# Optimization experiments

Measured on AMD Instinct MI355X. Metric: run time of the kernel, lower is better.

Reference implementation:

```python
import jax, jax.numpy as jnp
import numpy as np

V, D, H, L, S_MAX, FF = 32000, 1024, 16, 6, 1024, 4096
HD = D // H
EPS = 1e-5

def _ln(x, g, b):
    mu = jnp.mean(x, axis=-1, keepdims=True)
    var = jnp.mean((x - mu) ** 2, axis=-1, keepdims=True)
    return (x - mu) * jax.lax.rsqrt(var + EPS) * g + b

def setup_inputs() -> dict:
    key = jax.random.key(0)
    ks = jax.random.split(key, 12)
    std = 0.02
    d = {}
    d['x'] = jax.random.randint(ks[0], (2, 1024), 0, V)
    d['tok_emb'] = std * jax.random.normal(ks[1], (V, D), jnp.float32)
    d['pos_emb'] = std * jax.random.normal(ks[2], (S_MAX, D), jnp.float32)
    d['ln1_g'] = jnp.ones((L, D)); d['ln1_b'] = jnp.zeros((L, D))
    d['qkv_w'] = std * jax.random.normal(ks[3], (L, 3 * D, D), jnp.float32)
    d['qkv_b'] = jnp.zeros((L, 3 * D))
    d['proj_w'] = std * jax.random.normal(ks[4], (L, D, D), jnp.float32)
    d['proj_b'] = jnp.zeros((L, D))
    d['ln2_g'] = jnp.ones((L, D)); d['ln2_b'] = jnp.zeros((L, D))
    d['fc1_w'] = std * jax.random.normal(ks[5], (L, FF, D), jnp.float32)
    d['fc1_b'] = jnp.zeros((L, FF))
    d['fc2_w'] = std * jax.random.normal(ks[6], (L, D, FF), jnp.float32)
    d['fc2_b'] = jnp.zeros((L, D))
    d['lnf_g'] = jnp.ones((D,)); d['lnf_b'] = jnp.zeros((D,))
    d['head_w'] = std * jax.random.normal(ks[7], (V, D), jnp.float32)
    return d

def _gpt(x, tok_emb, pos_emb, ln1_g, ln1_b, qkv_w, qkv_b, proj_w, proj_b,
         ln2_g, ln2_b, fc1_w, fc1_b, fc2_w, fc2_b, lnf_g, lnf_b, head_w):
    B, S = x.shape
    h = tok_emb[x] + pos_emb[:S][None]  # (B,S,D)
    scale = HD ** -0.5
    causal = jnp.tril(jnp.ones((S, S), bool))
    neg_inf = jnp.finfo(h.dtype).min

    def block(h, p):
        l1g, l1b, qw, qb, pw, pb, l2g, l2b, f1w, f1b, f2w, f2b = p
        xn = _ln(h, l1g, l1b)
        qkv = xn @ qw.T + qb  # (B,S,3D)
        qkv = qkv.reshape(B, S, 3, H, HD).transpose(2, 0, 3, 1, 4)  # (3,B,H,S,HD)
        q, k, v = qkv[0], qkv[1], qkv[2]
        scores = jnp.einsum('bhqd,bhkd->bhqk', q, k) * scale
        scores = jnp.where(causal, scores, neg_inf)
        attn = jax.nn.softmax(scores, axis=-1)
        o = jnp.einsum('bhqk,bhkd->bhqd', attn, v)
        o = o.transpose(0, 2, 1, 3).reshape(B, S, D)
        h = h + (o @ pw.T + pb)
        xn = _ln(h, l2g, l2b)
        ff = jax.nn.gelu(xn @ f1w.T + f1b, approximate=False) @ f2w.T + f2b
        return h + ff, None

    params = (ln1_g, ln1_b, qkv_w, qkv_b, proj_w, proj_b,
              ln2_g, ln2_b, fc1_w, fc1_b, fc2_w, fc2_b)
    h, _ = jax.lax.scan(block, h, params)
    h = _ln(h, lnf_g, lnf_b)
    return h @ head_w.T  # (B,S,V)

def reference(x, tok_emb, pos_emb, ln1_g, ln1_b, qkv_w, qkv_b, proj_w, proj_b,
              ln2_g, ln2_b, fc1_w, fc1_b, fc2_w, fc2_b, lnf_g, lnf_b, head_w):
    return _gpt(x, tok_emb, pos_emb, ln1_g, ln1_b, qkv_w, qkv_b, proj_w, proj_b,
                ln2_g, ln2_b, fc1_w, fc1_b, fc2_w, fc2_b, lnf_g, lnf_b, head_w)
```

## Files before the change

kernel.cpp:

```cpp
#include <hip/hip_runtime.h>

typedef unsigned short u16;
typedef unsigned int   u32;
typedef __bf16 bf16x8 __attribute__((ext_vector_type(8)));
typedef float  f32x4  __attribute__((ext_vector_type(4)));

#define DEV __device__ __forceinline__

DEV u16 f2bf(float f) {
    u32 u = __builtin_bit_cast(u32, f);
    u32 r = u + 0x7FFFu + ((u >> 16) & 1u);
    return (u16)(r >> 16);
}

DEV void gload16(const void* g, void* l) {
    __builtin_amdgcn_global_load_lds((const __attribute__((address_space(1))) void*)g,
                                     (__attribute__((address_space(3))) void*)l, 16, 0, 0);
}

DEV int xcd_swz(int bid, int nwg) {
    int q = nwg >> 3, r = nwg & 7;
    int xcd = bid & 7, idx = bid >> 3;
    return (xcd < r ? xcd * (q + 1) : r * (q + 1) + (xcd - r) * q) + idx;
}

DEV int swz(int p) {
    int m = (((p >> 7) & 1) << 6) | (((p >> 9) & 1) << 5) | (((p >> 8) & 1) << 4);
    return p ^ m;
}

__global__ void cvt_k(const float* __restrict__ src, u16* __restrict__ dst, int n4) {
    int i = blockIdx.x * blockDim.x + threadIdx.x;
    int stride = gridDim.x * blockDim.x;
    for (; i < n4; i += stride) {
        float4 v = ((const float4*)src)[i];
        ushort4 u;
        u.x = f2bf(v.x); u.y = f2bf(v.y); u.z = f2bf(v.z); u.w = f2bf(v.w);
        ((ushort4*)dst)[i] = u;
    }
}

__global__ void cvt4_k(const float* __restrict__ s0, const float* __restrict__ s1,
                       const float* __restrict__ s2, const float* __restrict__ s3,
                       u16* __restrict__ dst, int n0, int n1, int n2, int n3) {
    int i = blockIdx.x * blockDim.x + threadIdx.x;
    int stride = gridDim.x * blockDim.x;
    int t0 = n0, t1 = t0 + n1, t2 = t1 + n2, t3 = t2 + n3;
    for (; i < t3; i += stride) {
        const float* s; int j;
        if (i < t0)      { s = s0; j = i; }
        else if (i < t1) { s = s1; j = i - t0; }
        else if (i < t2) { s = s2; j = i - t1; }
        else             { s = s3; j = i - t2; }
        float4 v = ((const float4*)s)[j];
        ushort4 u;
        u.x = f2bf(v.x); u.y = f2bf(v.y); u.z = f2bf(v.z); u.w = f2bf(v.w);
        ((ushort4*)dst)[i] = u;
    }
}

__global__ void embed_k(const int* __restrict__ x, const float* __restrict__ te,
                        const float* __restrict__ pe, float* __restrict__ h) {
    int row = blockIdx.x;
    int t = threadIdx.x;
    int tok = x[row];
    int s = row & 1023;
    float4 a = ((const float4*)(te + (size_t)tok * 1024))[t];
    float4 p = ((const float4*)(pe + (size_t)s * 1024))[t];
    a.x += p.x; a.y += p.y; a.z += p.z; a.w += p.w;
    ((float4*)(h + (size_t)row * 1024))[t] = a;
}

__global__ void ln_k(const float* __restrict__ in, const float* __restrict__ g,
                     const float* __restrict__ b, u16* __restrict__ out) {
    int row = blockIdx.x;
    int t = threadIdx.x;
    float4 v = ((const float4*)(in + (size_t)row * 1024))[t];
    float s = v.x + v.y + v.z + v.w;
    float s2 = v.x * v.x + v.y * v.y + v.z * v.z + v.w * v.w;
    #pragma unroll
    for (int msk = 1; msk < 64; msk <<= 1) {
        s  += __shfl_xor(s, msk);
        s2 += __shfl_xor(s2, msk);
    }
    __shared__ float ps[4], ps2[4];
    if ((t & 63) == 0) { ps[t >> 6] = s; ps2[t >> 6] = s2; }
    __syncthreads();
    s = ps[0] + ps[1] + ps[2] + ps[3];
    s2 = ps2[0] + ps2[1] + ps2[2] + ps2[3];
    float mu = s * (1.0f / 1024.0f);
    float var = s2 * (1.0f / 1024.0f) - mu * mu;
    float rstd = rsqrtf(var + 1e-5f);
    float4 gg = ((const float4*)g)[t];
    float4 bb = ((const float4*)b)[t];
    ushort4 o;
    o.x = f2bf((v.x - mu) * rstd * gg.x + bb.x);
    o.y = f2bf((v.y - mu) * rstd * gg.y + bb.y);
    o.z = f2bf((v.z - mu) * rstd * gg.z + bb.z);
    o.w = f2bf((v.w - mu) * rstd * gg.w + bb.w);
    ((ushort4*)out)[(size_t)row * 256 + t] = o;
}

__global__ void fuse2_k(const float* __restrict__ p0, const float* __restrict__ p1,
                        const float* __restrict__ bias, float* __restrict__ h) {
    int row = blockIdx.x;
    int t = threadIdx.x;
    size_t idx = (size_t)row * 256 + t;
    float4 a = ((const float4*)p0)[idx];
    float4 b = ((const float4*)p1)[idx];
    float4 c = ((const float4*)bias)[t];
    float4 v = ((const float4*)h)[idx];
    v.x += a.x + b.x + c.x;
    v.y += a.y + b.y + c.y;
    v.z += a.z + b.z + c.z;
    v.w += a.w + b.w + c.w;
    ((float4*)h)[idx] = v;
}

template<int PH>
DEV void phase_mma(const bf16x8 (&af)[2][2], const bf16x8 (&bfr)[4][2], f32x4 (&acc)[8][4]) {
    __builtin_amdgcn_s_barrier();
    asm volatile("s_waitcnt lgkmcnt(0)" ::: "memory");
    __builtin_amdgcn_sched_barrier(0);
    __builtin_amdgcn_s_setprio(1);
    #pragma unroll
    for (int ms = 0; ms < 2; ++ms)
        #pragma unroll
        for (int nj = 0; nj < 4; ++nj)
            #pragma unroll
            for (int kk = 0; kk < 2; ++kk)
                acc[PH * 2 + ms][nj] = __builtin_amdgcn_mfma_f32_16x16x32_bf16(
                    af[ms][kk], bfr[nj][kk], acc[PH * 2 + ms][nj], 0, 0, 0);
    __builtin_amdgcn_s_setprio(0);
}

template<int PH>
DEV void read_afrags(const char* Ab, int arow, int fr, int fq, bf16x8 (&af)[2][2]) {
    #pragma unroll
    for (int ms = 0; ms < 2; ++ms)
        #pragma unroll
        for (int kk = 0; kk < 2; ++kk) {
            int lin = (arow + (PH * 2 + ms) * 16 + fr) * 128 + kk * 64 + fq * 16;
            af[ms][kk] = *(const bf16x8*)(Ab + swz(lin));
        }
}

template<int BIAS, int OUTBF>
__global__ __launch_bounds__(512, 2)
void gemm8p(const u16* __restrict__ A, const u16* __restrict__ Bw,
            const float* __restrict__ bias,
            float* __restrict__ outf, u16* __restrict__ outb,
            int M, int N, int K) {
    __shared__ char lds[131072];
    char* ldsA = lds;
    char* ldsB = lds + 65536;
    const int t = threadIdx.x;
    const int w = t >> 6, l = t & 63;
    const int fr = l & 15, fq = l >> 4;
    const int wm = w >> 2, wn = w & 3;

    int bid = blockIdx.y * gridDim.x + blockIdx.x;
    int swzb = xcd_swz(bid, gridDim.x * gridDim.y);
    const int m0 = (swzb % gridDim.x) * 256;
    const int n0 = (swzb / gridDim.x) * 256;
    const int nt = K >> 6;
    const int arow = wm * 128;

    const u16* Asrc = A + (size_t)m0 * K;
    const u16* Bsrc = Bw + (size_t)n0 * K;

    size_t o00, o01, o10, o11;
    {
        int p;
        p = 0 * 16384 + 0 * 8192 + t * 16; o00 = (size_t)(p >> 7) * K + ((swz(p) & 127) >> 1);
        p = 0 * 16384 + 1 * 8192 + t * 16; o01 = (size_t)(p >> 7) * K + ((swz(p) & 127) >> 1);
        p = 1 * 16384 + 0 * 8192 + t * 16; o10 = (size_t)(p >> 7) * K + ((swz(p) & 127) >> 1);
        p = 1 * 16384 + 1 * 8192 + t * 16; o11 = (size_t)(p >> 7) * K + ((swz(p) & 127) >> 1);
    }
    const int wb = w * 1024;

    gload16(Asrc + o00, ldsA + wb);
    gload16(Asrc + o01, ldsA + 8192 + wb);
    gload16(Asrc + o10, ldsA + 16384 + wb);
    gload16(Asrc + o11, ldsA + 16384 + 8192 + wb);
    gload16(Bsrc + o00, ldsB + wb);
    gload16(Bsrc + o01, ldsB + 8192 + wb);
    gload16(Bsrc + o10, ldsB + 16384 + wb);
    gload16(Bsrc + o11, ldsB + 16384 + 8192 + wb);
    gload16(Bsrc + o00 + 64, ldsB + 32768 + wb);
    gload16(Bsrc + o01 + 64, ldsB + 32768 + 8192 + wb);
    gload16(Bsrc + o10 + 64, ldsB + 32768 + 16384 + wb);
    gload16(Bsrc + o11 + 64, ldsB + 32768 + 16384 + 8192 + wb);
    asm volatile("s_waitcnt vmcnt(4)" ::: "memory");
    __builtin_amdgcn_s_barrier();
    __builtin_amdgcn_sched_barrier(0);

    f32x4 acc[8][4] = {};

    for (int T = 0; T < nt; ++T) {
        const char* Ab = ldsA + (T & 1) * 32768;
        const char* Bb = ldsB + (T & 1) * 32768;
        char* Anx = ldsA + ((T + 1) & 1) * 32768;
        char* Bnx = ldsB + (T & 1) * 32768;
        const bool stA = (T + 1 < nt), stB = (T + 2 < nt);
        const size_t kA = (size_t)(T + 1) * 64, kB = (size_t)(T + 2) * 64;

        bf16x8 bfr[4][2], af[2][2];

        #pragma unroll
        for (int nj = 0; nj < 4; ++nj)
            #pragma unroll
            for (int kk = 0; kk < 2; ++kk) {
                int lin = (wn * 64 + nj * 16 + fr) * 128 + kk * 64 + fq * 16;
                bfr[nj][kk] = *(const bf16x8*)(Bb + swz(lin));
            }
        read_afrags<0>(Ab, arow, fr, fq, af);
        if (stA) {
            gload16(Asrc + o00 + kA, Anx + wb);
            gload16(Asrc + o01 + kA, Anx + 8192 + wb);
        }
        phase_mma<0>(af, bfr, acc);
        __builtin_amdgcn_s_barrier();

        read_afrags<1>(Ab, arow, fr, fq, af);
        if (stA) {
            gload16(Asrc + o10 + kA, Anx + 16384 + wb);
            gload16(Asrc + o11 + kA, Anx + 16384 + 8192 + wb);
        }
        phase_mma<1>(af, bfr, acc);
        __builtin_amdgcn_s_barrier();

        read_afrags<2>(Ab, arow, fr, fq, af);
        if (stB) {
            gload16(Bsrc + o00 + kB, Bnx + wb);
            gload16(Bsrc + o01 + kB, Bnx + 8192 + wb);
        }
        phase_mma<2>(af, bfr, acc);
        __builtin_amdgcn_s_barrier();

        read_afrags<3>(Ab, arow, fr, fq, af);
        if (stB) {
            gload16(Bsrc + o10 + kB, Bnx + 16384 + wb);
            gload16(Bsrc + o11 + kB, Bnx + 16384 + 8192 + wb);
        }
        phase_mma<3>(af, bfr, acc);
        if (stB)      asm volatile("s_waitcnt vmcnt(4)" ::: "memory");
        else if (stA) asm volatile("s_waitcnt vmcnt(0)" ::: "memory");
        __builtin_amdgcn_s_barrier();
        __builtin_amdgcn_sched_barrier(0);
    }

    #pragma unroll
    for (int mi = 0; mi < 8; ++mi) {
        #pragma unroll
        for (int nj = 0; nj < 4; ++nj) {
            #pragma unroll
            for (int r = 0; r < 4; ++r) {
                int row = m0 + wm * 128 + mi * 16 + fq * 4 + r;
                int col = n0 + wn * 64 + nj * 16 + fr;
                float v = acc[mi][nj][r];
                if (BIAS) v += bias[col];
                if (OUTBF) outb[(size_t)row * N + col] = f2bf(v);
                else       outf[(size_t)row * N + col] = v;
            }
        }
    }
}

template<int BM, int BN, int BIAS, int GELU_, int RES, int OUTBF, int SPLITK>
__global__ void gemm_db(const u16* __restrict__ A, const u16* __restrict__ Bw,
                        const float* __restrict__ bias, const float* __restrict__ res,
                        float* __restrict__ outf, u16* __restrict__ outb,
                        int M, int N, int K) {
    constexpr int MR = BM / 32;
    constexpr int NR = BN / 32;
    constexpr int AL = BM / 64;
    constexpr int BL = BN / 64;
    __shared__ u16 lA[2][BM * 32];
    __shared__ u16 lB[2][BN * 32];
    const int t = threadIdx.x;
    const int w = t >> 6, l = t & 63;

    int bid = blockIdx.y * gridDim.x + blockIdx.x;
    int swzb = xcd_swz(bid, gridDim.x * gridDim.y);
    const int m0 = (swzb % gridDim.x) * BM;
    const int n0 = (swzb / gridDim.x) * BN;

    int kbase = 0, Keff = K;
    if (SPLITK) { Keff = K >> 1; kbase = blockIdx.z * Keff; }
    const int nt = Keff >> 5;

    const int wr = (w >> 1) * (BM / 2), wc = (w & 1) * (BN / 2);
    const int fr = l & 15, fq = l >> 4;
    const int g0 = w * 64 + l;

    const int srow = g0 >> 2, scol = (g0 & 3) * 8;

    f32x4 acc[MR][NR] = {};

    #pragma unroll
    for (int i = 0; i < AL; ++i)
        gload16(A + (size_t)(m0 + srow + i * 64) * K + kbase + scol, lA[0] + (srow + i * 64) * 32 + scol);
    #pragma unroll
    for (int i = 0; i < BL; ++i)
        gload16(Bw + (size_t)(n0 + srow + i * 64) * K + kbase + scol, lB[0] + (srow + i * 64) * 32 + scol);
    __syncthreads();

    for (int T = 0; T < nt; ++T) {
        const int cur = T & 1, nxt = cur ^ 1;
        if (T + 1 < nt) {
            const int kk = kbase + (T + 1) * 32;
            #pragma unroll
            for (int i = 0; i < AL; ++i)
                gload16(A + (size_t)(m0 + srow + i * 64) * K + kk + scol, lA[nxt] + (srow + i * 64) * 32 + scol);
            #pragma unroll
            for (int i = 0; i < BL; ++i)
                gload16(Bw + (size_t)(n0 + srow + i * 64) * K + kk + scol, lB[nxt] + (srow + i * 64) * 32 + scol);
        }
        bf16x8 af[MR], bfv[NR];
        #pragma unroll
        for (int mi = 0; mi < MR; ++mi)
            af[mi] = *(const bf16x8*)(lA[cur] + (wr + mi * 16 + fr) * 32 + fq * 8);
        #pragma unroll
        for (int ni = 0; ni < NR; ++ni)
            bfv[ni] = *(const bf16x8*)(lB[cur] + (wc + ni * 16 + fr) * 32 + fq * 8);
        #pragma unroll
        for (int mi = 0; mi < MR; ++mi)
            #pragma unroll
            for (int ni = 0; ni < NR; ++ni)
                acc[mi][ni] = __builtin_amdgcn_mfma_f32_16x16x32_bf16(af[mi], bfv[ni], acc[mi][ni], 0, 0, 0);
        __syncthreads();
    }

    float* op = outf;
    if (SPLITK) op = outf + (size_t)blockIdx.z * M * N;

    #pragma unroll
    for (int mi = 0; mi < MR; ++mi) {
        #pragma unroll
        for (int ni = 0; ni < NR; ++ni) {
            #pragma unroll
            for (int r = 0; r < 4; ++r) {
                int row = m0 + wr + mi * 16 + fq * 4 + r;
                int col = n0 + wc + ni * 16 + fr;
                float v = acc[mi][ni][r];
                if (BIAS) v += bias[col];
                if (GELU_) v = 0.5f * v * (1.0f + erff(v * 0.70710678118f));
                if (RES) v += res[(size_t)row * N + col];
                if (OUTBF) outb[(size_t)row * N + col] = f2bf(v);
                else       op[(size_t)row * N + col] = v;
            }
        }
    }
}

__global__ void attn_k(const u16* __restrict__ qkv, u16* __restrict__ o) {
    __shared__ u16 lK[64 * 64];
    __shared__ u16 lV[64 * 64];
    __shared__ u16 lP[4 * 16 * 64];
    const int t = threadIdx.x;
    const int w = t >> 6, l = t & 63;
    const int fr = l & 15, fq = l >> 4;

    int swzb = xcd_swz(blockIdx.x, gridDim.x);
    const int qb = 15 - (swzb & 15);
    const int hh = (swzb >> 4) & 15;
    const int b  = swzb >> 8;
    const int q0 = qb * 64;

    const u16* srcK[2];
    #pragma unroll
    for (int i = 0; i < 2; ++i) {
        int p = (t + i * 256) * 16;
        int L = swz(p);
        srcK[i] = qkv + ((size_t)(b * 1024) + (L >> 7)) * 3072 + 1024 + hh * 64 + ((L & 127) >> 1);
    }

    bf16x8 qf[2];
    {
        size_t base = ((size_t)(b * 1024) + q0 + w * 16 + fr) * 3072 + hh * 64;
        qf[0] = *(const bf16x8*)(qkv + base + fq * 8);
        qf[1] = *(const bf16x8*)(qkv + base + 32 + fq * 8);
    }

    float m_run[4], l_run[4];
    f32x4 acc_o[4] = {};
    #pragma unroll
    for (int r = 0; r < 4; ++r) { m_run[r] = -__builtin_inff(); l_run[r] = 0.0f; }

    for (int kv0 = 0; kv0 <= q0; kv0 += 64) {
        #pragma unroll
        for (int i = 0; i < 2; ++i)
            gload16(srcK[i] + (size_t)kv0 * 3072, (char*)lK + w * 1024 + i * 4096);
        #pragma unroll
        for (int i = 0; i < 2; ++i) {
            int g = t + i * 256;
            int kv = g >> 3, d0 = (g & 7) * 8;
            const u32* gv = (const u32*)(qkv + ((size_t)(b * 1024) + kv0 + kv) * 3072 + 2048 + hh * 64 + d0);
            u32 v0 = gv[0], v1 = gv[1], v2 = gv[2], v3 = gv[3];
            u16 e[8] = { (u16)v0, (u16)(v0 >> 16), (u16)v1, (u16)(v1 >> 16),
                         (u16)v2, (u16)(v2 >> 16), (u16)v3, (u16)(v3 >> 16) };
            #pragma unroll
            for (int j = 0; j < 8; ++j) {
                int pv = ((d0 + j) * 64 + kv) * 2;
                *(u16*)((char*)lV + swz(pv)) = e[j];
            }
        }
        __syncthreads();

        f32x4 accs[4] = {};
        #pragma unroll
        for (int nt = 0; nt < 4; ++nt) {
            #pragma unroll
            for (int ks = 0; ks < 2; ++ks) {
                int pk = ((nt * 16 + fr) * 64 + ks * 32 + fq * 8) * 2;
                bf16x8 kf = *(const bf16x8*)((const char*)lK + swz(pk));
                accs[nt] = __builtin_amdgcn_mfma_f32_16x16x32_bf16(qf[ks], kf, accs[nt], 0, 0, 0);
            }
        }

        float p[4][4], mx[4], rs[4];
        #pragma unroll
        for (int r = 0; r < 4; ++r) {
            int qg = q0 + w * 16 + fq * 4 + r;
            float m = -__builtin_inff();
            #pragma unroll
            for (int nt = 0; nt < 4; ++nt) {
                int kvg = kv0 + nt * 16 + fr;
                float s = (kvg <= qg) ? accs[nt][r] * 0.125f : -__builtin_inff();
                p[nt][r] = s;
                m = fmaxf(m, s);
            }
            mx[r] = m;
        }
        #pragma unroll
        for (int msk = 1; msk < 16; msk <<= 1) {
            #pragma unroll
            for (int r = 0; r < 4; ++r) mx[r] = fmaxf(mx[r], __shfl_xor(mx[r], msk));
        }
        float mnew[4], alpha[4];
        #pragma unroll
        for (int r = 0; r < 4; ++r) {
            mnew[r] = fmaxf(m_run[r], mx[r]);
            alpha[r] = __expf(m_run[r] - mnew[r]);
            float s = 0.0f;
            #pragma unroll
            for (int nt = 0; nt < 4; ++nt) {
                float pv = __expf(p[nt][r] - mnew[r]);
                p[nt][r] = pv;
                s += pv;
            }
            rs[r] = s;
        }
        #pragma unroll
        for (int msk = 1; msk < 16; msk <<= 1) {
            #pragma unroll
            for (int r = 0; r < 4; ++r) rs[r] += __shfl_xor(rs[r], msk);
        }
        #pragma unroll
        for (int r = 0; r < 4; ++r) {
            l_run[r] = l_run[r] * alpha[r] + rs[r];
            m_run[r] = mnew[r];
        }
        #pragma unroll
        for (int nt = 0; nt < 4; ++nt)
            #pragma unroll
            for (int r = 0; r < 4; ++r) acc_o[nt][r] *= alpha[r];

        #pragma unroll
        for (int nt = 0; nt < 4; ++nt)
            #pragma unroll
            for (int r = 0; r < 4; ++r) {
                int pp = (w * 1024 + (fq * 4 + r) * 64 + nt * 16 + fr) * 2;
                *(u16*)((char*)lP + swz(pp)) = f2bf(p[nt][r]);
            }
        __syncthreads();

        bf16x8 pa[2];
        #pragma unroll
        for (int ks = 0; ks < 2; ++ks) {
            int ppr = (w * 1024 + fr * 64 + ks * 32 + fq * 8) * 2;
            pa[ks] = *(const bf16x8*)((const char*)lP + swz(ppr));
        }
        #pragma unroll
        for (int nt = 0; nt < 4; ++nt) {
            #pragma unroll
            for (int ks = 0; ks < 2; ++ks) {
                int pvr = ((nt * 16 + fr) * 64 + ks * 32 + fq * 8) * 2;
                bf16x8 vf = *(const bf16x8*)((const char*)lV + swz(pvr));
                acc_o[nt] = __builtin_amdgcn_mfma_f32_16x16x32_bf16(pa[ks], vf, acc_o[nt], 0, 0, 0);
            }
        }
        __syncthreads();
    }

    #pragma unroll
    for (int nt = 0; nt < 4; ++nt) {
        #pragma unroll
        for (int r = 0; r < 4; ++r) {
            int qg = q0 + w * 16 + fq * 4 + r;
            int d = nt * 16 + fr;
            float ov = acc_o[nt][r] / l_run[r];
            o[((size_t)(b * 1024) + qg) * 1024 + hh * 64 + d] = f2bf(ov);
        }
    }
}

extern "C" void kernel_launch(void* const* d_in, const int* in_sizes, int n_in,
                              void* d_out, int out_size, void* d_ws, size_t ws_size,
                              hipStream_t stream) {
    const int*   x       = (const int*)  d_in[0];
    const float* tok_emb = (const float*)d_in[1];
    const float* pos_emb = (const float*)d_in[2];
    const float* ln1_g   = (const float*)d_in[3];
    const float* ln1_b   = (const float*)d_in[4];
    const float* qkv_w   = (const float*)d_in[5];
    const float* qkv_b   = (const float*)d_in[6];
    const float* proj_w  = (const float*)d_in[7];
    const float* proj_b  = (const float*)d_in[8];
    const float* ln2_g   = (const float*)d_in[9];
    const float* ln2_b   = (const float*)d_in[10];
    const float* fc1_w   = (const float*)d_in[11];
    const float* fc1_b   = (const float*)d_in[12];
    const float* fc2_w   = (const float*)d_in[13];
    const float* fc2_b   = (const float*)d_in[14];
    const float* lnf_g   = (const float*)d_in[15];
    const float* lnf_b   = (const float*)d_in[16];
    const float* head_w  = (const float*)d_in[17];
    float* out = (float*)d_out;

    char* ws = (char*)d_ws;
    float* h   = (float*)(ws + 0);
    u16*   xn  = (u16*)(ws + 8388608);
    u16*   qkv = (u16*)(ws + 12582912);
    u16*   ob  = (u16*)(ws + 25165824);
    u16*   ff  = (u16*)(ws + 29360128);
    u16*   wq  = (u16*)(ws + 46137344);
    float* pbuf = (float*)(ws + 12582912);

    u16* wqkv = wq;
    u16* wproj = wqkv + 3072 * 1024;
    u16* wfc1  = wproj + 1024 * 1024;
    u16* wfc2  = wfc1 + 4096 * 1024;

    const int M = 2048;

    embed_k<<<dim3(2048), 256, 0, stream>>>(x, tok_emb, pos_emb, h);

    for (int lyr = 0; lyr < 6; ++lyr) {
        cvt4_k<<<dim3(2048), 256, 0, stream>>>(
            qkv_w + (size_t)lyr * 3072 * 1024, proj_w + (size_t)lyr * 1024 * 1024,
            fc1_w + (size_t)lyr * 4096 * 1024, fc2_w + (size_t)lyr * 1024 * 4096,
            wq, 3072 * 256, 1024 * 256, 4096 * 256, 4096 * 256);
        ln_k<<<dim3(2048), 256, 0, stream>>>(h, ln1_g + lyr * 1024, ln1_b + lyr * 1024, xn);
        gemm_db<128, 64, 1, 0, 0, 1, 0><<<dim3(16, 48), 256, 0, stream>>>(
            xn, wqkv, qkv_b + lyr * 3072, nullptr, nullptr, qkv, M, 3072, 1024);
        attn_k<<<dim3(512), 256, 0, stream>>>(qkv, ob);
        gemm_db<64, 64, 1, 0, 1, 0, 0><<<dim3(32, 16), 256, 0, stream>>>(
            ob, wproj, proj_b + lyr * 1024, h, h, nullptr, M, 1024, 1024);
        ln_k<<<dim3(2048), 256, 0, stream>>>(h, ln2_g + lyr * 1024, ln2_b + lyr * 1024, xn);
        gemm_db<128, 64, 1, 1, 0, 1, 0><<<dim3(16, 64), 256, 0, stream>>>(
            xn, wfc1, fc1_b + lyr * 4096, nullptr, nullptr, ff, M, 4096, 1024);
        gemm_db<128, 64, 0, 0, 0, 0, 1><<<dim3(16, 16, 2), 256, 0, stream>>>(
            ff, wfc2, nullptr, nullptr, pbuf, nullptr, M, 1024, 4096);
        fuse2_k<<<dim3(2048), 256, 0, stream>>>(
            pbuf, pbuf + (size_t)M * 1024, fc2_b + lyr * 1024, h);
    }

    ln_k<<<dim3(2048), 256, 0, stream>>>(h, lnf_g, lnf_b, xn);
    cvt_k<<<dim3(2048), 256, 0, stream>>>(head_w, wq, 32000 * 1024 / 4);
    gemm8p<0, 0><<<dim3(8, 125), 512, 0, stream>>>(
        xn, wq, nullptr, out, nullptr, M, 32000, 1024);
}
```

Before: 1.336 ms.

## Add 128x128 eight-wave pipelined GEMM for QKV/FC layers; widen attention query tile

Adds a new 512-thread GEMM kernel with 128x128 tiles, staged A/B prefetch through LDS, and MFMA priority hints. It replaces the 128x64 double-buffered GEMM for the QKV, FC1 and split-K FC2 projections, cutting per-tile operand reloads and grid size. The attention kernel now processes 128 query rows per block with 8 waves sharing each K/V tile load, and masks out inactive waves on the diagonal. The gain comes from better data reuse, at the cost of fewer blocks and some idle waves on causal boundary tiles.

```diff
diff --git a/kernel.cpp b/kernel.cpp
--- a/kernel.cpp
+++ b/kernel.cpp
@@ -267,6 +267,145 @@
     }
 }
 
+template<int BIAS, int GELU_, int OUTBF, int SPLITK>
+__global__ __launch_bounds__(512, 2)
+void gemm4p(const u16* __restrict__ A, const u16* __restrict__ Bw,
+            const float* __restrict__ bias,
+            float* __restrict__ outf, u16* __restrict__ outb,
+            int M, int N, int K) {
+    __shared__ char lds[65536];
+    char* ldsA = lds;
+    char* ldsB = lds + 32768;
+    const int t = threadIdx.x;
+    const int w = t >> 6, l = t & 63;
+    const int fr = l & 15, fq = l >> 4;
+    const int wm = w >> 2, wn = w & 3;
+
+    int bid = blockIdx.y * gridDim.x + blockIdx.x;
+    int swzb = xcd_swz(bid, gridDim.x * gridDim.y);
+    const int m0 = (swzb % gridDim.x) * 128;
+    const int n0 = (swzb / gridDim.x) * 128;
+
+    int kbase = 0, Keff = K;
+    if (SPLITK) { Keff = K >> 1; kbase = blockIdx.z * Keff; }
+    const int nt = Keff >> 6;
+
+    const u16* Asrc = A + (size_t)m0 * K + kbase;
+    const u16* Bsrc = Bw + (size_t)n0 * K + kbase;
+
+    size_t o0, o1;
+    {
+        int p = t * 16;        o0 = (size_t)(p >> 7) * K + ((swz(p) & 127) >> 1);
+        p = 8192 + t * 16;     o1 = (size_t)(p >> 7) * K + ((swz(p) & 127) >> 1);
+    }
+    const int wb = w * 1024;
+
+    gload16(Asrc + o0, ldsA + wb);
+    gload16(Asrc + o1, ldsA + 8192 + wb);
+    gload16(Bsrc + o0, ldsB + wb);
+    gload16(Bsrc + o1, ldsB + 8192 + wb);
+    gload16(Bsrc + o0 + 64, ldsB + 16384 + wb);
+    gload16(Bsrc + o1 + 64, ldsB + 16384 + 8192 + wb);
+    asm volatile("s_waitcnt vmcnt(2)" ::: "memory");
+    __builtin_amdgcn_s_barrier();
+    __builtin_amdgcn_sched_barrier(0);
+
+    f32x4 acc[4][2] = {};
+
+    for (int T = 0; T < nt; ++T) {
+        const char* Ab = ldsA + (T & 1) * 16384;
+        const char* Bb = ldsB + (T & 1) * 16384;
+        char* Anx = ldsA + ((T + 1) & 1) * 16384;
+        char* Bnx = ldsB + (T & 1) * 16384;
+        const bool stA = (T + 1 < nt), stB = (T + 2 < nt);
+        const size_t kA = (size_t)(T + 1) * 64, kB = (size_t)(T + 2) * 64;
+
+        bf16x8 bfr[2][2], af[2][2];
+
+        #pragma unroll
+        for (int nj = 0; nj < 2; ++nj)
+            #pragma unroll
+            for (int kk = 0; kk < 2; ++kk) {
+                int lin = (wn * 32 + nj * 16 + fr) * 128 + kk * 64 + fq * 16;
+                bfr[nj][kk] = *(const bf16x8*)(Bb + swz(lin));
+            }
+        #pragma unroll
+        for (int ms = 0; ms < 2; ++ms)
+            #pragma unroll
+            for (int kk = 0; kk < 2; ++kk) {
+                int lin = (wm * 64 + ms * 16 + fr) * 128 + kk * 64 + fq * 16;
+                af[ms][kk] = *(const bf16x8*)(Ab + swz(lin));
+            }
+        if (stA) {
+            gload16(Asrc + o0 + kA, Anx + wb);
+            gload16(Asrc + o1 + kA, Anx + 8192 + wb);
+        }
+        __builtin_amdgcn_s_barrier();
+        asm volatile("s_waitcnt lgkmcnt(0)" ::: "memory");
+        __builtin_amdgcn_sched_barrier(0);
+        __builtin_amdgcn_s_setprio(1);
+        #pragma unroll
+        for (int ms = 0; ms < 2; ++ms)
+            #pragma unroll
+            for (int nj = 0; nj < 2; ++nj)
+                #pragma unroll
+                for (int kk = 0; kk < 2; ++kk)
+                    acc[ms][nj] = __builtin_amdgcn_mfma_f32_16x16x32_bf16(
+                        af[ms][kk], bfr[nj][kk], acc[ms][nj], 0, 0, 0);
+        __builtin_amdgcn_s_setprio(0);
+        __builtin_amdgcn_s_barrier();
+
+        #pragma unroll
+        for (int ms = 0; ms < 2; ++ms)
+            #pragma unroll
+            for (int kk = 0; kk < 2; ++kk) {
+                int lin = (wm * 64 + (2 + ms) * 16 + fr) * 128 + kk * 64 + fq * 16;
+                af[ms][kk] = *(const bf16x8*)(Ab + swz(lin));
+            }
+        if (stB) {
+            gload16(Bsrc + o0 + kB, Bnx + wb);
+            gload16(Bsrc + o1 + kB, Bnx + 8192 + wb);
+        }
+        __builtin_amdgcn_s_barrier();
+        asm volatile("s_waitcnt lgkmcnt(0)" ::: "memory");
+        __builtin_amdgcn_sched_barrier(0);
+        __builtin_amdgcn_s_setprio(1);
+        #pragma unroll
+        for (int ms = 0; ms < 2; ++ms)
+            #pragma unroll
+            for (int nj = 0; nj < 2; ++nj)
+                #pragma unroll
+                for (int kk = 0; kk < 2; ++kk)
+                    acc[2 + ms][nj] = __builtin_amdgcn_mfma_f32_16x16x32_bf16(
+                        af[ms][kk], bfr[nj][kk], acc[2 + ms][nj], 0, 0, 0);
+        __builtin_amdgcn_s_setprio(0);
+        if (stB)      asm volatile("s_waitcnt vmcnt(2)" ::: "memory");
+        else if (stA) asm volatile("s_waitcnt vmcnt(0)" ::: "memory");
+        __builtin_amdgcn_s_barrier();
+        __builtin_amdgcn_sched_barrier(0);
+    }
+
+    float* op = outf;
+    if (SPLITK) op = outf + (size_t)blockIdx.z * M * N;
+
+    #pragma unroll
+    for (int mi = 0; mi < 4; ++mi) {
+        #pragma unroll
+        for (int nj = 0; nj < 2; ++nj) {
+            #pragma unroll
+            for (int r = 0; r < 4; ++r) {
+                int row = m0 + wm * 64 + mi * 16 + fq * 4 + r;
+                int col = n0 + wn * 32 + nj * 16 + fr;
+                float v = acc[mi][nj][r];
+                if (BIAS) v += bias[col];
+                if (GELU_) v = 0.5f * v * (1.0f + erff(v * 0.70710678118f));
+                if (OUTBF) outb[(size_t)row * N + col] = f2bf(v);
+                else       op[(size_t)row * N + col] = v;
+            }
+        }
+    }
+}
+
 template<int BM, int BN, int BIAS, int GELU_, int RES, int OUTBF, int SPLITK>
 __global__ void gemm_db(const u16* __restrict__ A, const u16* __restrict__ Bw,
                         const float* __restrict__ bias, const float* __restrict__ res,
@@ -354,31 +493,32 @@
     }
 }
 
-__global__ void attn_k(const u16* __restrict__ qkv, u16* __restrict__ o) {
+__global__ __launch_bounds__(512, 2)
+void attn_k(const u16* __restrict__ qkv, u16* __restrict__ o) {
     __shared__ u16 lK[64 * 64];
     __shared__ u16 lV[64 * 64];
-    __shared__ u16 lP[4 * 16 * 64];
+    __shared__ u16 lP[8 * 16 * 64];
     const int t = threadIdx.x;
     const int w = t >> 6, l = t & 63;
     const int fr = l & 15, fq = l >> 4;
 
     int swzb = xcd_swz(blockIdx.x, gridDim.x);
-    const int qb = 15 - (swzb & 15);
-    const int hh = (swzb >> 4) & 15;
-    const int b  = swzb >> 8;
-    const int q0 = qb * 64;
-
-    const u16* srcK[2];
-    #pragma unroll
-    for (int i = 0; i < 2; ++i) {
-        int p = (t + i * 256) * 16;
+    const int qb = 7 - (swzb & 7);
+    const int hh = (swzb >> 3) & 15;
+    const int b  = swzb >> 7;
+    const int q0 = qb * 128;
+    const int qw = q0 + w * 16;
+
+    const u16* srcK;
+    {
+        int p = t * 16;
         int L = swz(p);
-        srcK[i] = qkv + ((size_t)(b * 1024) + (L >> 7)) * 3072 + 1024 + hh * 64 + ((L & 127) >> 1);
+        srcK = qkv + ((size_t)(b * 1024) + (L >> 7)) * 3072 + 1024 + hh * 64 + ((L & 127) >> 1);
     }
 
     bf16x8 qf[2];
     {
-        size_t base = ((size_t)(b * 1024) + q0 + w * 16 + fr) * 3072 + hh * 64;
+        size_t base = ((size_t)(b * 1024) + qw + fr) * 3072 + hh * 64;
         qf[0] = *(const bf16x8*)(qkv + base + fq * 8);
         qf[1] = *(const bf16x8*)(qkv + base + 32 + fq * 8);
     }
@@ -388,14 +528,10 @@
     #pragma unroll
     for (int r = 0; r < 4; ++r) { m_run[r] = -__builtin_inff(); l_run[r] = 0.0f; }
 
-    for (int kv0 = 0; kv0 <= q0; kv0 += 64) {
-        #pragma unroll
-        for (int i = 0; i < 2; ++i)
-            gload16(srcK[i] + (size_t)kv0 * 3072, (char*)lK + w * 1024 + i * 4096);
-        #pragma unroll
-        for (int i = 0; i < 2; ++i) {
-            int g = t + i * 256;
-            int kv = g >> 3, d0 = (g & 7) * 8;
+    for (int kv0 = 0; kv0 < q0 + 128; kv0 += 64) {
+        gload16(srcK + (size_t)kv0 * 3072, (char*)lK + w * 1024);
+        {
+            int kv = t >> 3, d0 = (t & 7) * 8;
             const u32* gv = (const u32*)(qkv + ((size_t)(b * 1024) + kv0 + kv) * 3072 + 2048 + hh * 64 + d0);
             u32 v0 = gv[0], v1 = gv[1], v2 = gv[2], v3 = gv[3];
             u16 e[8] = { (u16)v0, (u16)(v0 >> 16), (u16)v1, (u16)(v1 >> 16),
@@ -408,97 +544,99 @@
         }
         __syncthreads();
 
-        f32x4 accs[4] = {};
-        #pragma unroll
-        for (int nt = 0; nt < 4; ++nt) {
+        const bool active = (kv0 <= qw + 15);
+        if (active) {
+            f32x4 accs[4] = {};
+            #pragma unroll
+            for (int nt = 0; nt < 4; ++nt) {
+                #pragma unroll
+                for (int ks = 0; ks < 2; ++ks) {
+                    int pk = ((nt * 16 + fr) * 64 + ks * 32 + fq * 8) * 2;
+                    bf16x8 kf = *(const bf16x8*)((const char*)lK + swz(pk));
+                    accs[nt] = __builtin_amdgcn_mfma_f32_16x16x32_bf16(qf[ks], kf, accs[nt], 0, 0, 0);
+                }
+            }
+
+            float p[4][4], mx[4], rs[4];
+            #pragma unroll
+            for (int r = 0; r < 4; ++r) {
+                int qg = qw + fq * 4 + r;
+                float m = -__builtin_inff();
+                #pragma unroll
+                for (int nt = 0; nt < 4; ++nt) {
+                    int kvg = kv0 + nt * 16 + fr;
+                    float s = (kvg <= qg) ? accs[nt][r] * 0.125f : -__builtin_inff();
+                    p[nt][r] = s;
+                    m = fmaxf(m, s);
+                }
+                mx[r] = m;
+            }
+            #pragma unroll
+            for (int msk = 1; msk < 16; msk <<= 1) {
+                #pragma unroll
+                for (int r = 0; r < 4; ++r) mx[r] = fmaxf(mx[r], __shfl_xor(mx[r], msk));
+            }
+            float mnew[4], alpha[4];
+            #pragma unroll
+            for (int r = 0; r < 4; ++r) {
+                mnew[r] = fmaxf(m_run[r], mx[r]);
+                alpha[r] = __expf(m_run[r] - mnew[r]);
+                float s = 0.0f;
+                #pragma unroll
+                for (int nt = 0; nt < 4; ++nt) {
+                    float pv = __expf(p[nt][r] - mnew[r]);
+                    p[nt][r] = pv;
+                    s += pv;
+                }
+                rs[r] = s;
+            }
+            #pragma unroll
+            for (int msk = 1; msk < 16; msk <<= 1) {
+                #pragma unroll
+                for (int r = 0; r < 4; ++r) rs[r] += __shfl_xor(rs[r], msk);
+            }
+            #pragma unroll
+            for (int r = 0; r < 4; ++r) {
+                l_run[r] = l_run[r] * alpha[r] + rs[r];
+                m_run[r] = mnew[r];
+            }
+            #pragma unroll
+            for (int nt = 0; nt < 4; ++nt)
+                #pragma unroll
+                for (int r = 0; r < 4; ++r) acc_o[nt][r] *= alpha[r];
+
+            #pragma unroll
+            for (int nt = 0; nt < 4; ++nt)
+                #pragma unroll
+                for (int r = 0; r < 4; ++r) {
+                    int pp = (w * 1024 + (fq * 4 + r) * 64 + nt * 16 + fr) * 2;
+                    *(u16*)((char*)lP + swz(pp)) = f2bf(p[nt][r]);
+                }
+
+            bf16x8 pa[2];
             #pragma unroll
             for (int ks = 0; ks < 2; ++ks) {
-                int pk = ((nt * 16 + fr) * 64 + ks * 32 + fq * 8) * 2;
-                bf16x8 kf = *(const bf16x8*)((const char*)lK + swz(pk));
-                accs[nt] = __builtin_amdgcn_mfma_f32_16x16x32_bf16(qf[ks], kf, accs[nt], 0, 0, 0);
-            }
-        }
-
-        float p[4][4], mx[4], rs[4];
+                int ppr = (w * 1024 + fr * 64 + ks * 32 + fq * 8) * 2;
+                pa[ks] = *(const bf16x8*)((const char*)lP + swz(ppr));
+            }
+            #pragma unroll
+            for (int nt = 0; nt < 4; ++nt) {
+                #pragma unroll
+                for (int ks = 0; ks < 2; ++ks) {
+                    int pvr = ((nt * 16 + fr) * 64 + ks * 32 + fq * 8) * 2;
+                    bf16x8 vf = *(const bf16x8*)((const char*)lV + swz(pvr));
+                    acc_o[nt] = __builtin_amdgcn_mfma_f32_16x16x32_bf16(pa[ks], vf, acc_o[nt], 0, 0, 0);
+                }
+            }
+        }
+        __syncthreads();
+    }
+
+    #pragma unroll
+    for (int nt = 0; nt < 4; ++nt) {
         #pragma unroll
         for (int r = 0; r < 4; ++r) {
-            int qg = q0 + w * 16 + fq * 4 + r;
-            float m = -__builtin_inff();
-            #pragma unroll
-            for (int nt = 0; nt < 4; ++nt) {
-                int kvg = kv0 + nt * 16 + fr;
-                float s = (kvg <= qg) ? accs[nt][r] * 0.125f : -__builtin_inff();
-                p[nt][r] = s;
-                m = fmaxf(m, s);
-            }
-            mx[r] = m;
-        }
-        #pragma unroll
-        for (int msk = 1; msk < 16; msk <<= 1) {
-            #pragma unroll
-            for (int r = 0; r < 4; ++r) mx[r] = fmaxf(mx[r], __shfl_xor(mx[r], msk));
-        }
-        float mnew[4], alpha[4];
-        #pragma unroll
-        for (int r = 0; r < 4; ++r) {
-            mnew[r] = fmaxf(m_run[r], mx[r]);
-            alpha[r] = __expf(m_run[r] - mnew[r]);
-            float s = 0.0f;
-            #pragma unroll
-            for (int nt = 0; nt < 4; ++nt) {
-                float pv = __expf(p[nt][r] - mnew[r]);
-                p[nt][r] = pv;
-                s += pv;
-            }
-            rs[r] = s;
-        }
-        #pragma unroll
-        for (int msk = 1; msk < 16; msk <<= 1) {
-            #pragma unroll
-            for (int r = 0; r < 4; ++r) rs[r] += __shfl_xor(rs[r], msk);
-        }
-        #pragma unroll
-        for (int r = 0; r < 4; ++r) {
-            l_run[r] = l_run[r] * alpha[r] + rs[r];
-            m_run[r] = mnew[r];
-        }
-        #pragma unroll
-        for (int nt = 0; nt < 4; ++nt)
-            #pragma unroll
-            for (int r = 0; r < 4; ++r) acc_o[nt][r] *= alpha[r];
-
-        #pragma unroll
-        for (int nt = 0; nt < 4; ++nt)
-            #pragma unroll
-            for (int r = 0; r < 4; ++r) {
-                int pp = (w * 1024 + (fq * 4 + r) * 64 + nt * 16 + fr) * 2;
-                *(u16*)((char*)lP + swz(pp)) = f2bf(p[nt][r]);
-            }
-        __syncthreads();
-
-        bf16x8 pa[2];
-        #pragma unroll
-        for (int ks = 0; ks < 2; ++ks) {
-            int ppr = (w * 1024 + fr * 64 + ks * 32 + fq * 8) * 2;
-            pa[ks] = *(const bf16x8*)((const char*)lP + swz(ppr));
-        }
-        #pragma unroll
-        for (int nt = 0; nt < 4; ++nt) {
-            #pragma unroll
-            for (int ks = 0; ks < 2; ++ks) {
-                int pvr = ((nt * 16 + fr) * 64 + ks * 32 + fq * 8) * 2;
-                bf16x8 vf = *(const bf16x8*)((const char*)lV + swz(pvr));
-                acc_o[nt] = __builtin_amdgcn_mfma_f32_16x16x32_bf16(pa[ks], vf, acc_o[nt], 0, 0, 0);
-            }
-        }
-        __syncthreads();
-    }
-
-    #pragma unroll
-    for (int nt = 0; nt < 4; ++nt) {
-        #pragma unroll
-        for (int r = 0; r < 4; ++r) {
-            int qg = q0 + w * 16 + fq * 4 + r;
+            int qg = qw + fq * 4 + r;
             int d = nt * 16 + fr;
             float ov = acc_o[nt][r] / l_run[r];
             o[((size_t)(b * 1024) + qg) * 1024 + hh * 64 + d] = f2bf(ov);
@@ -553,16 +691,16 @@
             fc1_w + (size_t)lyr * 4096 * 1024, fc2_w + (size_t)lyr * 1024 * 4096,
             wq, 3072 * 256, 1024 * 256, 4096 * 256, 4096 * 256);
         ln_k<<<dim3(2048), 256, 0, stream>>>(h, ln1_g + lyr * 1024, ln1_b + lyr * 1024, xn);
-        gemm_db<128, 64, 1, 0, 0, 1, 0><<<dim3(16, 48), 256, 0, stream>>>(
-            xn, wqkv, qkv_b + lyr * 3072, nullptr, nullptr, qkv, M, 3072, 1024);
-        attn_k<<<dim3(512), 256, 0, stream>>>(qkv, ob);
+        gemm4p<1, 0, 1, 0><<<dim3(16, 24), 512, 0, stream>>>(
+            xn, wqkv, qkv_b + lyr * 3072, nullptr, qkv, M, 3072, 1024);
+        attn_k<<<dim3(256), 512, 0, stream>>>(qkv, ob);
         gemm_db<64, 64, 1, 0, 1, 0, 0><<<dim3(32, 16), 256, 0, stream>>>(
             ob, wproj, proj_b + lyr * 1024, h, h, nullptr, M, 1024, 1024);
         ln_k<<<dim3(2048), 256, 0, stream>>>(h, ln2_g + lyr * 1024, ln2_b + lyr * 1024, xn);
-        gemm_db<128, 64, 1, 1, 0, 1, 0><<<dim3(16, 64), 256, 0, stream>>>(
-            xn, wfc1, fc1_b + lyr * 4096, nullptr, nullptr, ff, M, 4096, 1024);
-        gemm_db<128, 64, 0, 0, 0, 0, 1><<<dim3(16, 16, 2), 256, 0, stream>>>(
-            ff, wfc2, nullptr, nullptr, pbuf, nullptr, M, 1024, 4096);
+        gemm4p<1, 1, 1, 0><<<dim3(16, 32), 512, 0, stream>>>(
+            xn, wfc1, fc1_b + lyr * 4096, nullptr, ff, M, 4096, 1024);
+        gemm4p<0, 0, 0, 1><<<dim3(16, 8, 2), 512, 0, stream>>>(
+            ff, wfc2, nullptr, pbuf, nullptr, M, 1024, 4096);
         fuse2_k<<<dim3(2048), 256, 0, stream>>>(
             pbuf, pbuf + (size_t)M * 1024, fc2_b + lyr * 1024, h);
     }
```

After: 1.256 ms. 1.06x faster.
